# Kernel optimization log

Measured on AMD Instinct MI355X. Metric: run time of the kernel, lower is better.

## Reference

```python
import jax, jax.numpy as jnp
import numpy as np

E = 512
H = 8
HD = E // H
EPS = 1e-5


def setup_inputs() -> dict:
    key = jax.random.key(0)
    ks = jax.random.split(key, 12)
    S, B = 2048, 4
    bound_in = float(np.sqrt(6.0 / (3 * E + E)))  # xavier_uniform for in_proj
    inp = {
        "x": jax.random.normal(ks[0], (S, B, E), dtype=jnp.float32),
        "in_proj_weight": jax.random.uniform(ks[1], (3 * E, E), minval=-bound_in, maxval=bound_in, dtype=jnp.float32),
        "in_proj_bias": jnp.zeros((3 * E,), jnp.float32),
        "out_proj_weight": jax.random.normal(ks[2], (E, E), dtype=jnp.float32) * 0.02,
        "out_proj_bias": jnp.zeros((E,), jnp.float32),
        "ln1_gamma": jnp.ones((E,), jnp.float32),
        "ln1_beta": jnp.zeros((E,), jnp.float32),
        "fc1_weight": jax.random.normal(ks[3], (4 * E, E), dtype=jnp.float32) * 0.02,
        "fc1_bias": jnp.zeros((4 * E,), jnp.float32),
        "fc2_weight": jax.random.normal(ks[4], (E, 4 * E), dtype=jnp.float32) * 0.02,
        "fc2_bias": jnp.zeros((E,), jnp.float32),
        "ln2_gamma": jnp.ones((E,), jnp.float32),
        "ln2_beta": jnp.zeros((E,), jnp.float32),
    }
    return inp


def _layer_norm(x, gamma, beta):
    mu = jnp.mean(x, axis=-1, keepdims=True)
    var = jnp.mean(jnp.square(x - mu), axis=-1, keepdims=True)
    return (x - mu) * jax.lax.rsqrt(var + EPS) * gamma + beta


def _encoder_layer(x, in_w, in_b, out_w, out_b, g1, b1, fc1_w, fc1_b, fc2_w, fc2_b, g2, b2):
    S, B, _ = x.shape
    # --- self attention (hand-rolled, full S x S scores as in original) ---
    qkv = x @ in_w.T + in_b                      # [S, B, 3E]
    q, k, v = jnp.split(qkv, 3, axis=-1)         # each [S, B, E]
    # [S, B, E] -> [B*H, S, HD]
    def to_heads(t):
        return t.reshape(S, B * H, HD).transpose(1, 0, 2)
    q, k, v = to_heads(q), to_heads(k), to_heads(v)
    scores = jnp.einsum('bsd,btd->bst', q, k) / jnp.sqrt(jnp.float32(HD))  # [B*H, S, S]
    attn_w = jax.nn.softmax(scores, axis=-1)
    attn = jnp.einsum('bst,btd->bsd', attn_w, v)  # [B*H, S, HD]
    attn = attn.transpose(1, 0, 2).reshape(S, B, E)
    attn = attn @ out_w.T + out_b
    # --- residual + LN ---
    x = _layer_norm(x + attn, g1, b1)
    # --- FFN ---
    h = jax.nn.relu(x @ fc1_w.T + fc1_b)
    h = h @ fc2_w.T + fc2_b
    return _layer_norm(x + h, g2, b2)


def reference(x, in_proj_weight, in_proj_bias, out_proj_weight, out_proj_bias,
              ln1_gamma, ln1_beta, fc1_weight, fc1_bias, fc2_weight, fc2_bias,
              ln2_gamma, ln2_beta):
    return _encoder_layer(x, in_proj_weight, in_proj_bias, out_proj_weight, out_proj_bias,
                          ln1_gamma, ln1_beta, fc1_weight, fc1_bias, fc2_weight, fc2_bias,
                          ln2_gamma, ln2_beta)
```

## Files before the change

kernel.cpp:

```cpp
#include <hip/hip_runtime.h>

typedef _Float16 half8 __attribute__((ext_vector_type(8)));
typedef _Float16 half4 __attribute__((ext_vector_type(4)));
typedef float f32x4 __attribute__((ext_vector_type(4)));

static __device__ __forceinline__ f32x4 mfma16(half8 a, half8 b, f32x4 c) {
    return __builtin_amdgcn_mfma_f32_16x16x32_f16(a, b, c, 0, 0, 0);
}

static __device__ __forceinline__ void gload16(const void* g, const void* l) {
    __builtin_amdgcn_global_load_lds(
        (const __attribute__((address_space(1))) unsigned int*)(unsigned long long)g,
        (__attribute__((address_space(3))) unsigned int*)(unsigned int)(unsigned long long)l,
        16, 0, 0);
}

__global__ void __launch_bounds__(256) conv_all(const float* __restrict__ x,
                                                const float* __restrict__ inw,
                                                const float* __restrict__ outw,
                                                const float* __restrict__ f1w,
                                                const float* __restrict__ f2w,
                                                _Float16* __restrict__ X16,
                                                _Float16* __restrict__ WIN,
                                                _Float16* __restrict__ WOUT,
                                                _Float16* __restrict__ WF1,
                                                _Float16* __restrict__ WF2) {
    const int bid = blockIdx.x;
    const float* src;
    _Float16* dst;
    long base;
    if (bid < 2048)      { src = x;    dst = X16;  base = (long)bid * 2048; }
    else if (bid < 2432) { src = inw;  dst = WIN;  base = (long)(bid - 2048) * 2048; }
    else if (bid < 2560) { src = outw; dst = WOUT; base = (long)(bid - 2432) * 2048; }
    else if (bid < 3072) { src = f1w;  dst = WF1;  base = (long)(bid - 2560) * 2048; }
    else                 { src = f2w;  dst = WF2;  base = (long)(bid - 3072) * 2048; }
    const long i = base + threadIdx.x * 8;
    f32x4 v0 = *(const f32x4*)(src + i);
    f32x4 v1 = *(const f32x4*)(src + i + 4);
    half8 h;
#pragma unroll
    for (int j = 0; j < 4; j++) { h[j] = (_Float16)v0[j]; h[4 + j] = (_Float16)v1[j]; }
    *(half8*)(dst + i) = h;
}

template <int MODE, int NI>
__global__ void __launch_bounds__(256) gemm_bt(const _Float16* __restrict__ A,
                                               const _Float16* __restrict__ Bw,
                                               const float* __restrict__ bias,
                                               const float* __restrict__ resid,
                                               void* __restrict__ Cout,
                                               int M, int N, int K) {
    constexpr int BN = 32 * NI;
    __shared__ __align__(16) _Float16 As[2][128 * 32];
    __shared__ __align__(16) _Float16 Bs[2][BN * 32];
    const int tid = threadIdx.x;
    const int lane = tid & 63;
    const int w = tid >> 6;
    const int g = lane >> 4, l15 = lane & 15;
    const int wm = w >> 1, wn = w & 1;
    const long rowblk = (long)blockIdx.y * 128;
    const long colblk = (long)blockIdx.x * BN;

    const int lrow = lane >> 2;
    const int lcol = (lane & 3) * 8;

    f32x4 zero = {0.f, 0.f, 0.f, 0.f};
    f32x4 acc[4][NI];
#pragma unroll
    for (int i = 0; i < 4; i++)
#pragma unroll
        for (int j = 0; j < NI; j++) acc[i][j] = zero;

    auto stage = [&](int k0, int buf) {
        gload16(A + (rowblk + w * 32 + lrow) * (long)K + k0 + lcol, As[buf] + w * 1024);
        gload16(A + (rowblk + w * 32 + 16 + lrow) * (long)K + k0 + lcol, As[buf] + w * 1024 + 512);
#pragma unroll
        for (int c = 0; c < NI / 2; c++)
            gload16(Bw + (colblk + w * (8 * NI) + c * 16 + lrow) * (long)K + k0 + lcol,
                    Bs[buf] + w * (8 * NI) * 32 + c * 512);
    };

    stage(0, 0);
    int buf = 0;
    for (int k0 = 0; k0 < K; k0 += 32) {
        if (k0 + 32 < K) {
            stage(k0 + 32, buf ^ 1);
            if constexpr (NI == 4) asm volatile("s_waitcnt vmcnt(4)" ::: "memory");
            else                   asm volatile("s_waitcnt vmcnt(3)" ::: "memory");
        } else {
            asm volatile("s_waitcnt vmcnt(0)" ::: "memory");
        }
        __builtin_amdgcn_s_barrier();
        half8 af[4], bf[NI];
#pragma unroll
        for (int mi = 0; mi < 4; mi++)
            af[mi] = *(const half8*)(As[buf] + (wm * 64 + mi * 16 + l15) * 32 + g * 8);
#pragma unroll
        for (int ni = 0; ni < NI; ni++)
            bf[ni] = *(const half8*)(Bs[buf] + (wn * (16 * NI) + ni * 16 + l15) * 32 + g * 8);
#pragma unroll
        for (int mi = 0; mi < 4; mi++)
#pragma unroll
            for (int ni = 0; ni < NI; ni++)
                acc[mi][ni] = mfma16(bf[ni], af[mi], acc[mi][ni]);
        __builtin_amdgcn_s_barrier();
        buf ^= 1;
    }

#pragma unroll
    for (int mi = 0; mi < 4; mi++) {
        const long m = rowblk + wm * 64 + mi * 16 + l15;
#pragma unroll
        for (int ni = 0; ni < NI; ni++) {
            const long n0 = colblk + wn * (16 * NI) + ni * 16 + g * 4;
            const f32x4 bb = *(const f32x4*)(bias + n0);
            f32x4 v = acc[mi][ni] + bb;
            if (MODE == 1) {
#pragma unroll
                for (int r = 0; r < 4; r++) v[r] = fmaxf(v[r], 0.f);
            }
            if (MODE == 2) {
                const f32x4 rv = *(const f32x4*)(resid + m * N + n0);
                *(f32x4*)((float*)Cout + m * N + n0) = v + rv;
            } else if (MODE == 3) {
                const long sel = n0 >> 9;
                const int hh = (int)(n0 >> 6) & 7;
                const int d0 = (int)n0 & 63;
                const int ss = (int)(m >> 2), b = (int)m & 3;
                if (sel == 0) v *= 0.18033688f;
                half4 hv;
#pragma unroll
                for (int r = 0; r < 4; r++) hv[r] = (_Float16)v[r];
                *(half4*)((_Float16*)Cout + sel * (32L * 2048 * 64) +
                          ((long)(b * 8 + hh) * 2048 + ss) * 64 + d0) = hv;
            } else {
                half4 hv;
#pragma unroll
                for (int r = 0; r < 4; r++) hv[r] = (_Float16)v[r];
                *(half4*)((_Float16*)Cout + m * N + n0) = hv;
            }
        }
    }
    (void)M;
}

__global__ void __launch_bounds__(256) transpose_v(const _Float16* __restrict__ Vh,
                                                   _Float16* __restrict__ Vt) {
    __shared__ _Float16 T[64][72];
    const int tid = threadIdx.x;
    const int bh = blockIdx.y;
    const int t0 = blockIdx.x * 64;
    const _Float16* src = Vh + ((long)bh * 2048 + t0) * 64;
    const int row = tid >> 2, col = (tid & 3) * 16;
    *(half8*)&T[row][col] = *(const half8*)(src + row * 64 + col);
    *(half8*)&T[row][col + 8] = *(const half8*)(src + row * 64 + col + 8);
    __syncthreads();
    const int d = tid >> 2, tc = (tid & 3) * 16;
    half8 a, b;
#pragma unroll
    for (int j = 0; j < 8; j++) { a[j] = T[tc + j][d]; b[j] = T[tc + 8 + j][d]; }
    _Float16* dst = Vt + ((long)bh * 64 + d) * 2048 + t0 + tc;
    *(half8*)dst = a;
    *(half8*)(dst + 8) = b;
}

__global__ void __launch_bounds__(256) attn_fwd(const _Float16* __restrict__ Qh,
                                                const _Float16* __restrict__ Kh,
                                                const _Float16* __restrict__ Vt,
                                                _Float16* __restrict__ out) {
    __shared__ __align__(16) _Float16 Klds[2][64 * 64];
    __shared__ __align__(16) _Float16 Vlds[2][64 * 64];
    __shared__ __align__(16) _Float16 Plds[4][16 * 64];
    const int tid = threadIdx.x;
    const int lane = tid & 63;
    const int w = tid >> 6;
    const int g = lane >> 4, l15 = lane & 15;
    const int bh = blockIdx.y;
    const int b = bh >> 3, h = bh & 7;
    const int s0 = blockIdx.x * 64 + w * 16;
    const _Float16* Qb = Qh + (long)bh * 2048 * 64;
    const _Float16* Kb = Kh + (long)bh * 2048 * 64;
    const _Float16* Vb = Vt + (long)bh * 64 * 2048;

    const int srow = lane >> 3;
    const int scolb = (lane & 7) * 16;

    half8 qb[2];
#pragma unroll
    for (int ks = 0; ks < 2; ks++)
        qb[ks] = *(const half8*)(Qb + (s0 + l15) * 64 + ks * 32 + g * 8);

    f32x4 zero = {0.f, 0.f, 0.f, 0.f};
    f32x4 ot[4];
#pragma unroll
    for (int di = 0; di < 4; di++) ot[di] = zero;
    float lsum = 0.f;

    auto stage = [&](int t0, int buf) {
#pragma unroll
        for (int j = 0; j < 2; j++) {
            const int row = w * 16 + j * 8 + srow;
            const int src = scolb ^ ((row & 7) << 4);
            gload16(Kb + (long)(t0 + row) * 64 + (src >> 1),
                    Klds[buf] + (w * 16 + j * 8) * 64);
            gload16(Vb + (long)row * 2048 + t0 + (src >> 1),
                    Vlds[buf] + (w * 16 + j * 8) * 64);
        }
    };

    stage(0, 0);
    __syncthreads();
    int buf = 0;

    for (int t0 = 0; t0 < 2048; t0 += 64) {
        if (t0 + 64 < 2048) stage(t0 + 64, buf ^ 1);

        __builtin_amdgcn_s_setprio(1);
        f32x4 st[4];
#pragma unroll
        for (int ni = 0; ni < 4; ni++) {
            st[ni] = zero;
#pragma unroll
            for (int ks = 0; ks < 2; ks++) {
                const int t = ni * 16 + l15;
                const int cb = (ks * 64 + g * 16) ^ ((t & 7) << 4);
                half8 ka = *(const half8*)((const char*)Klds[buf] + t * 128 + cb);
                st[ni] = mfma16(ka, qb[ks], st[ni]);
            }
        }
        __builtin_amdgcn_s_setprio(0);

        char* const pw = (char*)Plds[w] + l15 * 128;
#pragma unroll
        for (int ni = 0; ni < 4; ni++) {
            half4 pv4;
#pragma unroll
            for (int r = 0; r < 4; r++) {
                const float pe = __builtin_exp2f(st[ni][r]);
                lsum += pe;
                pv4[r] = (_Float16)pe;
            }
            *(half4*)(pw + ((ni * 32 + g * 8) ^ ((l15 & 7) << 4))) = pv4;
        }

        half8 pa[2];
#pragma unroll
        for (int ks = 0; ks < 2; ks++)
            pa[ks] = *(const half8*)(pw + ((ks * 64 + g * 16) ^ ((l15 & 7) << 4)));
        __builtin_amdgcn_s_setprio(1);
#pragma unroll
        for (int di = 0; di < 4; di++)
#pragma unroll
            for (int ks = 0; ks < 2; ks++) {
                const int d = di * 16 + l15;
                const int cb = (ks * 64 + g * 16) ^ ((d & 7) << 4);
                half8 vb = *(const half8*)((const char*)Vlds[buf] + d * 128 + cb);
                ot[di] = mfma16(vb, pa[ks], ot[di]);
            }
        __builtin_amdgcn_s_setprio(0);

        __syncthreads();
        buf ^= 1;
    }

    lsum += __shfl_xor(lsum, 16);
    lsum += __shfl_xor(lsum, 32);
    const float inv = 1.f / lsum;
    const long q = s0 + l15;
#pragma unroll
    for (int di = 0; di < 4; di++) {
        half4 hv;
#pragma unroll
        for (int r = 0; r < 4; r++) hv[r] = (_Float16)(ot[di][r] * inv);
        *(half4*)(out + (q * 4 + b) * 512 + h * 64 + di * 16 + g * 4) = hv;
    }
}

__global__ void __launch_bounds__(256) ln_rows(const float* __restrict__ in,
                                               const float* __restrict__ gamma,
                                               const float* __restrict__ beta,
                                               float* __restrict__ outf,
                                               _Float16* __restrict__ outh) {
    const int tid = threadIdx.x, lane = tid & 63, w = tid >> 6;
    const long row = (long)blockIdx.x * 4 + w;
    const float* p = in + row * 512 + lane * 8;
    f32x4 v0 = *(const f32x4*)p;
    f32x4 v1 = *(const f32x4*)(p + 4);
    float s = v0[0] + v0[1] + v0[2] + v0[3] + v1[0] + v1[1] + v1[2] + v1[3];
    float q = v0[0] * v0[0] + v0[1] * v0[1] + v0[2] * v0[2] + v0[3] * v0[3] +
              v1[0] * v1[0] + v1[1] * v1[1] + v1[2] * v1[2] + v1[3] * v1[3];
#pragma unroll
    for (int off = 1; off < 64; off <<= 1) {
        s += __shfl_xor(s, off);
        q += __shfl_xor(q, off);
    }
    const float mu = s * (1.0f / 512.0f);
    const float var = q * (1.0f / 512.0f) - mu * mu;
    const float rstd = rsqrtf(var + 1e-5f);
    const float* gp = gamma + lane * 8;
    const float* bp = beta + lane * 8;
    f32x4 g0 = *(const f32x4*)gp, g1 = *(const f32x4*)(gp + 4);
    f32x4 b0 = *(const f32x4*)bp, b1 = *(const f32x4*)(bp + 4);
    f32x4 o0, o1;
#pragma unroll
    for (int j = 0; j < 4; j++) {
        o0[j] = (v0[j] - mu) * rstd * g0[j] + b0[j];
        o1[j] = (v1[j] - mu) * rstd * g1[j] + b1[j];
    }
    float* op = outf + row * 512 + lane * 8;
    *(f32x4*)op = o0;
    *(f32x4*)(op + 4) = o1;
    if (outh) {
        half8 hh;
#pragma unroll
        for (int j = 0; j < 4; j++) { hh[j] = (_Float16)o0[j]; hh[4 + j] = (_Float16)o1[j]; }
        *(half8*)(outh + row * 512 + lane * 8) = hh;
    }
}

extern "C" void kernel_launch(void* const* d_in, const int* in_sizes, int n_in,
                              void* d_out, int out_size, void* d_ws, size_t ws_size,
                              hipStream_t stream) {
    const float* x    = (const float*)d_in[0];
    const float* inw  = (const float*)d_in[1];
    const float* inb  = (const float*)d_in[2];
    const float* outw = (const float*)d_in[3];
    const float* outb = (const float*)d_in[4];
    const float* g1   = (const float*)d_in[5];
    const float* b1   = (const float*)d_in[6];
    const float* f1w  = (const float*)d_in[7];
    const float* f1b  = (const float*)d_in[8];
    const float* f2w  = (const float*)d_in[9];
    const float* f2b  = (const float*)d_in[10];
    const float* g2   = (const float*)d_in[11];
    const float* b2   = (const float*)d_in[12];

    char* ws = (char*)d_ws;
    const long MB = 1024 * 1024;
    _Float16* X16   = (_Float16*)(ws + 0);
    _Float16* HEADS = (_Float16*)(ws + 8 * MB);
    _Float16* H16   = (_Float16*)(ws + 0);
    _Float16* VT    = (_Float16*)(ws + 32 * MB);
    _Float16* ATT   = (_Float16*)(ws + 40 * MB);
    float*    PRE   = (float*)(ws + 48 * MB);
    float*    YF    = (float*)(ws + 64 * MB);
    _Float16* Y16   = (_Float16*)(ws + 80 * MB);
    _Float16* WIN   = (_Float16*)(ws + 88 * MB);
    _Float16* WOUT  = (_Float16*)(ws + 90 * MB);
    _Float16* WF1   = (_Float16*)(ws + 91 * MB);
    _Float16* WF2   = (_Float16*)(ws + 93 * MB);

    _Float16* Qh = HEADS;
    _Float16* Kh = HEADS + 32L * 2048 * 64;
    _Float16* Vh = HEADS + 2 * 32L * 2048 * 64;

    conv_all<<<3584, 256, 0, stream>>>(x, inw, outw, f1w, f2w, X16, WIN, WOUT, WF1, WF2);

    gemm_bt<3, 4><<<dim3(12, 64), 256, 0, stream>>>(X16, WIN, inb, nullptr, HEADS, 8192, 1536, 512);
    transpose_v<<<dim3(32, 32), 256, 0, stream>>>(Vh, VT);
    attn_fwd<<<dim3(32, 32), 256, 0, stream>>>(Qh, Kh, VT, ATT);
    gemm_bt<2, 2><<<dim3(8, 64), 256, 0, stream>>>(ATT, WOUT, outb, x, PRE, 8192, 512, 512);
    ln_rows<<<2048, 256, 0, stream>>>(PRE, g1, b1, YF, Y16);
    gemm_bt<1, 4><<<dim3(16, 64), 256, 0, stream>>>(Y16, WF1, f1b, nullptr, H16, 8192, 2048, 512);
    gemm_bt<2, 2><<<dim3(8, 64), 256, 0, stream>>>(H16, WF2, f2b, YF, PRE, 8192, 512, 2048);
    ln_rows<<<2048, 256, 0, stream>>>(PRE, g2, b2, (float*)d_out, nullptr);
}
```

Baseline: 305.1 us.

## Triple-buffer GEMM LDS staging and parametrize M tile for N=512 GEMMs

The GEMM now uses a three-stage LDS ring buffer that prefetches two K-steps ahead, with vmcnt waits computed per tile shape. The M tile is also made a template parameter so the two N=512 GEMMs (out-proj and FC2) use 64x64 tiles over a 128-row grid, doubling their block count. The goal is to hide more global-load latency and fill more CUs on the narrow GEMMs. The cost is extra LDS per block and smaller tiles with less reuse on those GEMMs.

```diff
diff --git a/kernel.cpp b/kernel.cpp
--- a/kernel.cpp
+++ b/kernel.cpp
@@ -13,6 +13,15 @@
         (const __attribute__((address_space(1))) unsigned int*)(unsigned long long)g,
         (__attribute__((address_space(3))) unsigned int*)(unsigned int)(unsigned long long)l,
         16, 0, 0);
+}
+
+template <int N> static __device__ __forceinline__ void waitcnt_vm() {
+    if constexpr (N == 0)      asm volatile("s_waitcnt vmcnt(0)" ::: "memory");
+    else if constexpr (N == 2) asm volatile("s_waitcnt vmcnt(2)" ::: "memory");
+    else if constexpr (N == 3) asm volatile("s_waitcnt vmcnt(3)" ::: "memory");
+    else if constexpr (N == 4) asm volatile("s_waitcnt vmcnt(4)" ::: "memory");
+    else if constexpr (N == 6) asm volatile("s_waitcnt vmcnt(6)" ::: "memory");
+    else if constexpr (N == 8) asm volatile("s_waitcnt vmcnt(8)" ::: "memory");
 }
 
 __global__ void __launch_bounds__(256) conv_all(const float* __restrict__ x,
@@ -43,73 +52,78 @@
     *(half8*)(dst + i) = h;
 }
 
-template <int MODE, int NI>
+template <int MODE, int MI, int NI>
 __global__ void __launch_bounds__(256) gemm_bt(const _Float16* __restrict__ A,
                                                const _Float16* __restrict__ Bw,
                                                const float* __restrict__ bias,
                                                const float* __restrict__ resid,
                                                void* __restrict__ Cout,
                                                int M, int N, int K) {
-    constexpr int BN = 32 * NI;
-    __shared__ __align__(16) _Float16 As[2][128 * 32];
-    __shared__ __align__(16) _Float16 Bs[2][BN * 32];
+    constexpr int L = MI / 2 + NI / 2;
+    __shared__ __align__(16) _Float16 As[3][32 * MI * 32];
+    __shared__ __align__(16) _Float16 Bs[3][32 * NI * 32];
     const int tid = threadIdx.x;
     const int lane = tid & 63;
     const int w = tid >> 6;
     const int g = lane >> 4, l15 = lane & 15;
     const int wm = w >> 1, wn = w & 1;
-    const long rowblk = (long)blockIdx.y * 128;
-    const long colblk = (long)blockIdx.x * BN;
+    const long rowblk = (long)blockIdx.y * (32 * MI);
+    const long colblk = (long)blockIdx.x * (32 * NI);
 
     const int lrow = lane >> 2;
     const int lcol = (lane & 3) * 8;
 
     f32x4 zero = {0.f, 0.f, 0.f, 0.f};
-    f32x4 acc[4][NI];
-#pragma unroll
-    for (int i = 0; i < 4; i++)
+    f32x4 acc[MI][NI];
+#pragma unroll
+    for (int i = 0; i < MI; i++)
 #pragma unroll
         for (int j = 0; j < NI; j++) acc[i][j] = zero;
 
-    auto stage = [&](int k0, int buf) {
-        gload16(A + (rowblk + w * 32 + lrow) * (long)K + k0 + lcol, As[buf] + w * 1024);
-        gload16(A + (rowblk + w * 32 + 16 + lrow) * (long)K + k0 + lcol, As[buf] + w * 1024 + 512);
+    auto stage = [&](int k0, int bufi) {
+#pragma unroll
+        for (int a = 0; a < MI / 2; a++)
+            gload16(A + (rowblk + w * (8 * MI) + a * 16 + lrow) * (long)K + k0 + lcol,
+                    As[bufi] + (w * (8 * MI) + a * 16) * 32);
 #pragma unroll
         for (int c = 0; c < NI / 2; c++)
             gload16(Bw + (colblk + w * (8 * NI) + c * 16 + lrow) * (long)K + k0 + lcol,
-                    Bs[buf] + w * (8 * NI) * 32 + c * 512);
+                    Bs[bufi] + (w * (8 * NI) + c * 16) * 32);
     };
 
     stage(0, 0);
-    int buf = 0;
+    if (32 < K) stage(32, 1);
+    int cur = 0;
     for (int k0 = 0; k0 < K; k0 += 32) {
-        if (k0 + 32 < K) {
-            stage(k0 + 32, buf ^ 1);
-            if constexpr (NI == 4) asm volatile("s_waitcnt vmcnt(4)" ::: "memory");
-            else                   asm volatile("s_waitcnt vmcnt(3)" ::: "memory");
+        if (k0 + 64 < K) {
+            int nxt = cur + 2; if (nxt >= 3) nxt -= 3;
+            stage(k0 + 64, nxt);
+            waitcnt_vm<2 * L>();
+        } else if (k0 + 32 < K) {
+            waitcnt_vm<L>();
         } else {
-            asm volatile("s_waitcnt vmcnt(0)" ::: "memory");
+            waitcnt_vm<0>();
         }
         __builtin_amdgcn_s_barrier();
-        half8 af[4], bf[NI];
-#pragma unroll
-        for (int mi = 0; mi < 4; mi++)
-            af[mi] = *(const half8*)(As[buf] + (wm * 64 + mi * 16 + l15) * 32 + g * 8);
+        half8 af[MI], bf[NI];
+#pragma unroll
+        for (int mi = 0; mi < MI; mi++)
+            af[mi] = *(const half8*)(As[cur] + (wm * (16 * MI) + mi * 16 + l15) * 32 + g * 8);
 #pragma unroll
         for (int ni = 0; ni < NI; ni++)
-            bf[ni] = *(const half8*)(Bs[buf] + (wn * (16 * NI) + ni * 16 + l15) * 32 + g * 8);
-#pragma unroll
-        for (int mi = 0; mi < 4; mi++)
+            bf[ni] = *(const half8*)(Bs[cur] + (wn * (16 * NI) + ni * 16 + l15) * 32 + g * 8);
+#pragma unroll
+        for (int mi = 0; mi < MI; mi++)
 #pragma unroll
             for (int ni = 0; ni < NI; ni++)
                 acc[mi][ni] = mfma16(bf[ni], af[mi], acc[mi][ni]);
         __builtin_amdgcn_s_barrier();
-        buf ^= 1;
-    }
-
-#pragma unroll
-    for (int mi = 0; mi < 4; mi++) {
-        const long m = rowblk + wm * 64 + mi * 16 + l15;
+        cur = (cur == 2) ? 0 : cur + 1;
+    }
+
+#pragma unroll
+    for (int mi = 0; mi < MI; mi++) {
+        const long m = rowblk + wm * (16 * MI) + mi * 16 + l15;
 #pragma unroll
         for (int ni = 0; ni < NI; ni++) {
             const long n0 = colblk + wn * (16 * NI) + ni * 16 + g * 4;
@@ -356,12 +370,12 @@
 
     conv_all<<<3584, 256, 0, stream>>>(x, inw, outw, f1w, f2w, X16, WIN, WOUT, WF1, WF2);
 
-    gemm_bt<3, 4><<<dim3(12, 64), 256, 0, stream>>>(X16, WIN, inb, nullptr, HEADS, 8192, 1536, 512);
+    gemm_bt<3, 4, 4><<<dim3(12, 64), 256, 0, stream>>>(X16, WIN, inb, nullptr, HEADS, 8192, 1536, 512);
     transpose_v<<<dim3(32, 32), 256, 0, stream>>>(Vh, VT);
     attn_fwd<<<dim3(32, 32), 256, 0, stream>>>(Qh, Kh, VT, ATT);
-    gemm_bt<2, 2><<<dim3(8, 64), 256, 0, stream>>>(ATT, WOUT, outb, x, PRE, 8192, 512, 512);
+    gemm_bt<2, 2, 2><<<dim3(8, 128), 256, 0, stream>>>(ATT, WOUT, outb, x, PRE, 8192, 512, 512);
     ln_rows<<<2048, 256, 0, stream>>>(PRE, g1, b1, YF, Y16);
-    gemm_bt<1, 4><<<dim3(16, 64), 256, 0, stream>>>(Y16, WF1, f1b, nullptr, H16, 8192, 2048, 512);
-    gemm_bt<2, 2><<<dim3(8, 64), 256, 0, stream>>>(H16, WF2, f2b, YF, PRE, 8192, 512, 2048);
+    gemm_bt<1, 4, 4><<<dim3(16, 64), 256, 0, stream>>>(Y16, WF1, f1b, nullptr, H16, 8192, 2048, 512);
+    gemm_bt<2, 2, 2><<<dim3(8, 128), 256, 0, stream>>>(H16, WF2, f2b, YF, PRE, 8192, 512, 2048);
     ln_rows<<<2048, 256, 0, stream>>>(PRE, g2, b2, (float*)d_out, nullptr);
 }
```

Measured after the change: 315.6 us. +3.5%, slower.
